# Kernel tuning notes

Measured on AMD Instinct MI355X. Metric: run time of the kernel, lower is better.

The kernel has to match this reference:

```python
import jax, jax.numpy as jnp
import numpy as np
from jax import lax

B, T, MEL, D, H, NC = 8, 256, 128, 192, 4, 20
C_EVENT, C_SCENE = 8, 64
ETA, LR, ALPHA = 0.9, 0.1, 0.01  # memory momentum, write lr, forget rate
EPS = 1e-5


def _ln(x, g, b):
    m = x.mean(-1, keepdims=True)
    v = ((x - m) ** 2).mean(-1, keepdims=True)
    return (x - m) / jnp.sqrt(v + EPS) * g + b


def _mem_step(x, t, M, S, Wk, Wv, Wq, chunk):
    # x: [B,D]; M,S: [B,D,D]. Titans-style neural memory, updated every `chunk` steps.
    k = x @ Wk
    v = x @ Wv
    q = x @ Wq
    err = v - jnp.einsum('bd,bde->be', k, M)          # surprise / prediction error
    S_new = ETA * S + LR * jnp.einsum('bd,be->bde', k, err)
    M_new = (1.0 - ALPHA) * M + S_new
    upd = (t % chunk) == 0
    S = jnp.where(upd, S_new, S)
    M = jnp.where(upd, M_new, M)
    out = jnp.einsum('bd,bde->be', q, M)              # retrieval
    return out, M, S


def setup_inputs() -> dict:
    key = jax.random.key(0)
    ks = jax.random.split(key, 24)
    w = lambda k, shp, s=0.05: jax.random.normal(k, shp, dtype=jnp.float32) * s
    inp = {
        'x': jax.random.normal(ks[0], (B, T, MEL), dtype=jnp.float32),
        'W_in': w(ks[1], (MEL, D)), 'b_in': jnp.zeros((D,), jnp.float32),
        # MHA at seq_len=1: softmax over one key -> weight 1, so only V and out proj matter
        'Wv_a': w(ks[2], (D, D)), 'bv_a': jnp.zeros((D,), jnp.float32),
        'Wo_a': w(ks[3], (D, D)), 'bo_a': jnp.zeros((D,), jnp.float32),
        # conformer conv module (degenerate seq_len=1: depthwise conv -> center tap)
        'ln1_g': jnp.ones((D,), jnp.float32), 'ln1_b': jnp.zeros((D,), jnp.float32),
        'pw1_w': w(ks[4], (D, 2 * D)), 'pw1_b': jnp.zeros((2 * D,), jnp.float32),
        'dw_w': w(ks[5], (D,), 0.2), 'dw_b': jnp.zeros((D,), jnp.float32),
        'bn_s': jnp.ones((D,), jnp.float32), 'bn_b': jnp.zeros((D,), jnp.float32),
        'pw2_w': w(ks[6], (D, D)), 'pw2_b': jnp.zeros((D,), jnp.float32),
        # theta (event) / delta (scene) neural memory projections
        'Wk_t': w(ks[7], (D, D)), 'Wv_t': w(ks[8], (D, D)), 'Wq_t': w(ks[9], (D, D)),
        'Wk_d': w(ks[10], (D, D)), 'Wv_d': w(ks[11], (D, D)), 'Wq_d': w(ks[12], (D, D)),
        'ln2_g': jnp.ones((D,), jnp.float32), 'ln2_b': jnp.zeros((D,), jnp.float32),
        'Wc': w(ks[13], (D, NC)), 'bc': jnp.zeros((NC,), jnp.float32),
    }
    return inp


def reference(x, W_in, b_in, Wv_a, bv_a, Wo_a, bo_a, ln1_g, ln1_b, pw1_w, pw1_b,
              dw_w, dw_b, bn_s, bn_b, pw2_w, pw2_b, Wk_t, Wv_t, Wq_t,
              Wk_d, Wv_d, Wq_d, ln2_g, ln2_b, Wc, bc):
    xp = x @ W_in + b_in                               # [B,T,D]

    def step(carry, inp):
        x_t, t = inp                                   # x_t: [B,D]
        Mt, St, Md, Sd = carry
        d_out, Md, Sd = _mem_step(x_t, t, Md, Sd, Wk_d, Wv_d, Wq_d, C_SCENE)
        x1 = x_t + 0.5 * d_out
        attn = (x1 @ Wv_a + bv_a) @ Wo_a + bo_a        # single-token self-attn
        x2 = x1 + attn
        h = _ln(x2, ln1_g, ln1_b)
        h = h @ pw1_w + pw1_b
        a, g = jnp.split(h, 2, axis=-1)
        h = a * jax.nn.sigmoid(g)                      # GLU
        h = h * dw_w + dw_b                            # depthwise conv center tap
        h = h * bn_s + bn_b                            # eval-mode BN
        h = jax.nn.silu(h)
        h = h @ pw2_w + pw2_b
        x3 = x2 + h
        t_out, Mt, St = _mem_step(x3, t, Mt, St, Wk_t, Wv_t, Wq_t, C_EVENT)
        x4 = x3 + 0.5 * t_out
        return (Mt, St, Md, Sd), _ln(x4, ln2_g, ln2_b)

    z = jnp.zeros((B, D, D), jnp.float32)
    xs = (jnp.swapaxes(xp, 0, 1), jnp.arange(T))       # [T,B,D], [T]
    _, ys = lax.scan(step, (z, z, z, z), xs)
    y = jnp.swapaxes(ys, 0, 1)                         # [B,T,D]
    pooled = y.mean(axis=1)
    return pooled @ Wc + bc                            # [B,NC]
```

## Files before the change

kernel.cpp:

```cpp
#include <hip/hip_runtime.h>
#include <math.h>

#define Bb 8
#define Tt 256
#define MEL 128
#define Dd 192
#define NCc 20
#define ND 4
#define NT 32
#define ETAc 0.9f
#define LRc 0.1f
#define MDEC 0.99f
#define EPSc 1e-5f
#define PT 2
#define PTILES 128
#define RTT 4
#define PADD 196

__device__ __forceinline__ float sigmoidf_(float x) {
    return 1.0f / (1.0f + __expf(-x));
}

__device__ __forceinline__ float memcoef(int n, int i) {
    float m = LRc, pw = LRc;
    for (int nn = i + 1; nn <= n; nn++) { pw *= ETAc; m = MDEC * m + pw; }
    return m;
}

__device__ __forceinline__ float dot4(float4 a, float4 b) {
    return a.x * b.x + a.y * b.y + a.z * b.z + a.w * b.w;
}

__global__ __launch_bounds__(192) void prep(
    const float* __restrict__ Wv_a, const float* __restrict__ Wo_a,
    const float* __restrict__ bv_a, const float* __restrict__ bo_a,
    const float* __restrict__ Wq_t, const float* __restrict__ Wq_d,
    const float* __restrict__ x, const float* __restrict__ W_in,
    const float* __restrict__ b_in, const float* __restrict__ Wk_d,
    const float* __restrict__ Wv_d,
    float* __restrict__ Wavo_ws, float* __restrict__ b_avo,
    float* __restrict__ WqtT, float* __restrict__ WqdT,
    float* __restrict__ Kd_ws, float* __restrict__ Vd_ws,
    float* __restrict__ pooled, unsigned int* __restrict__ cnt)
{
    __shared__ __align__(16) float smem[768];
    int blk = blockIdx.x, tid = threadIdx.x;

    if (blk < 48) {
        int m0 = blk * 4;
        for (int q = tid; q < 4 * Dd; q += 192) smem[q] = Wv_a[m0 * Dd + q];
        __syncthreads();
        int o = tid;
        float a0 = 0.f, a1 = 0.f, a2 = 0.f, a3 = 0.f;
        #pragma unroll 4
        for (int k = 0; k < Dd; k += 2) {
            float w0 = Wo_a[(k + 0) * Dd + o], w1 = Wo_a[(k + 1) * Dd + o];
            a0 += w0 * smem[0 * Dd + k] + w1 * smem[0 * Dd + k + 1];
            a1 += w0 * smem[1 * Dd + k] + w1 * smem[1 * Dd + k + 1];
            a2 += w0 * smem[2 * Dd + k] + w1 * smem[2 * Dd + k + 1];
            a3 += w0 * smem[3 * Dd + k] + w1 * smem[3 * Dd + k + 1];
        }
        Wavo_ws[(m0 + 0) * Dd + o] = a0;
        Wavo_ws[(m0 + 1) * Dd + o] = a1;
        Wavo_ws[(m0 + 2) * Dd + o] = a2;
        Wavo_ws[(m0 + 3) * Dd + o] = a3;
        return;
    }
    if (blk == 48) {
        int o = tid;
        float s = bo_a[o];
        #pragma unroll 4
        for (int m = 0; m < Dd; m++) s += bv_a[m] * Wo_a[m * Dd + o];
        b_avo[o] = s;
        return;
    }
    if (blk < 97) {
        int r0 = 4 * (blk - 49);
        float4 v;
        v.x = Wq_t[(r0 + 0) * Dd + tid];
        v.y = Wq_t[(r0 + 1) * Dd + tid];
        v.z = Wq_t[(r0 + 2) * Dd + tid];
        v.w = Wq_t[(r0 + 3) * Dd + tid];
        *(float4*)&WqtT[tid * Dd + r0] = v;
        return;
    }
    if (blk < 145) {
        int r0 = 4 * (blk - 97);
        float4 v;
        v.x = Wq_d[(r0 + 0) * Dd + tid];
        v.y = Wq_d[(r0 + 1) * Dd + tid];
        v.z = Wq_d[(r0 + 2) * Dd + tid];
        v.w = Wq_d[(r0 + 3) * Dd + tid];
        *(float4*)&WqdT[tid * Dd + r0] = v;
        return;
    }
    if (blk == 177) {
        for (int q = tid; q < Bb * Dd; q += 192) pooled[q] = 0.f;
        if (tid < 12) cnt[tid] = 0u;
        return;
    }

    int q = blk - 145;
    int b = q >> 2, i = q & 3;
    float* XR = smem;
    float* XP = smem + 128;
    if (tid < 128) XR[tid] = x[((size_t)b * Tt + 64 * i) * MEL + tid];
    __syncthreads();
    {
        int o = tid;
        float acc = b_in[o];
        #pragma unroll 8
        for (int k = 0; k < MEL; k += 4) {
            acc += W_in[(k + 0) * Dd + o] * XR[k + 0];
            acc += W_in[(k + 1) * Dd + o] * XR[k + 1];
            acc += W_in[(k + 2) * Dd + o] * XR[k + 2];
            acc += W_in[(k + 3) * Dd + o] * XR[k + 3];
        }
        XP[o] = acc;
    }
    __syncthreads();
    {
        int o = tid;
        float ak = 0.f, av = 0.f;
        #pragma unroll 4
        for (int k = 0; k < Dd; k += 4) {
            float x0 = XP[k + 0], x1 = XP[k + 1], x2 = XP[k + 2], x3 = XP[k + 3];
            ak += Wk_d[(k + 0) * Dd + o] * x0 + Wk_d[(k + 1) * Dd + o] * x1
                + Wk_d[(k + 2) * Dd + o] * x2 + Wk_d[(k + 3) * Dd + o] * x3;
            av += Wv_d[(k + 0) * Dd + o] * x0 + Wv_d[(k + 1) * Dd + o] * x1
                + Wv_d[(k + 2) * Dd + o] * x2 + Wv_d[(k + 3) * Dd + o] * x3;
        }
        Kd_ws[(b * ND + i) * Dd + o] = ak;
        Vd_ws[(b * ND + i) * Dd + o] = av;
    }
}

__global__ __launch_bounds__(192) void delta_solve(
    const float* __restrict__ WqdT, const float* __restrict__ Kd_ws,
    float* __restrict__ Vd_ws, float* __restrict__ Ud_ws)
{
    int blk = blockIdx.x, b = blk / 5, role = blk % 5, tid = threadIdx.x;
    if (role == 0) {
        __shared__ __align__(16) float K4[ND][Dd], V4[ND][Dd];
        __shared__ float G[16], mc[16];
        for (int q = tid; q < ND * 48; q += 192) {
            int i = q / 48, c = q - i * 48;
            ((float4*)K4[i])[c] = ((const float4*)&Kd_ws[(b * ND + i) * Dd])[c];
            ((float4*)V4[i])[c] = ((const float4*)&Vd_ws[(b * ND + i) * Dd])[c];
        }
        __syncthreads();
        if (tid < 16) {
            int i = tid >> 2, j = tid & 3;
            float s = 0.f;
            for (int d = 0; d < Dd; d++) s += K4[i][d] * K4[j][d];
            G[tid] = s;
            mc[tid] = (j <= i) ? memcoef(i, j) : 0.f;
        }
        __syncthreads();
        for (int i = 1; i < ND; i++) {
            float acc = V4[i][tid];
            for (int m = 0; m < i; m++)
                acc -= mc[(i - 1) * ND + m] * G[i * ND + m] * V4[m][tid];
            V4[i][tid] = acc;
            __syncthreads();
        }
        for (int i = 0; i < ND; i++) Vd_ws[(b * ND + i) * Dd + tid] = V4[i][tid];
    } else {
        __shared__ float KS[Dd];
        int i = role - 1;
        KS[tid] = Kd_ws[(b * ND + i) * Dd + tid];
        __syncthreads();
        int o = tid;
        float acc = 0.f;
        #pragma unroll 8
        for (int k = 0; k < Dd; k += 4) {
            acc += WqdT[(k + 0) * Dd + o] * KS[k + 0];
            acc += WqdT[(k + 1) * Dd + o] * KS[k + 1];
            acc += WqdT[(k + 2) * Dd + o] * KS[k + 2];
            acc += WqdT[(k + 3) * Dd + o] * KS[k + 3];
        }
        Ud_ws[(b * ND + i) * Dd + o] = acc;
    }
}

__global__ __launch_bounds__(192) void pipeline(
    const float* __restrict__ x, const float* __restrict__ W_in,
    const float* __restrict__ b_in,
    const float* __restrict__ ln1_g, const float* __restrict__ ln1_b,
    const float* __restrict__ pw1_w, const float* __restrict__ pw1_b,
    const float* __restrict__ dw_w, const float* __restrict__ dw_b,
    const float* __restrict__ bn_s, const float* __restrict__ bn_b,
    const float* __restrict__ pw2_w, const float* __restrict__ pw2_b,
    const float* __restrict__ Wavo_ws, const float* __restrict__ b_avo,
    const float* __restrict__ Ed_ws, const float* __restrict__ Ud_ws,
    float* __restrict__ x3_ws)
{
    int blk = blockIdx.x;
    int b = blk >> 7, tile = blk & 127;
    int t0 = tile * PT, n = tile >> 5;
    int tid = threadIdx.x;

    __shared__ __align__(16) float XR[PT][MEL];
    __shared__ __align__(16) float XP[PT][Dd];
    __shared__ __align__(16) float ED[ND][PADD], UD[ND][PADD];
    __shared__ __align__(16) float X1[PT][Dd], X2[PT][Dd];
    __shared__ __align__(16) float LNX[PT][Dd], HG[PT][Dd];
    __shared__ float WQs[PT * ND];
    __shared__ float mv[PT][2];

    if (tid < PT * 32) {
        int r = tid >> 5, c = tid & 31;
        ((float4*)XR[r])[c] = ((const float4*)&x[((size_t)b * Tt + t0 + r) * MEL])[c];
    }
    for (int q = tid; q < ND * 48 * 2; q += 192) {
        int which = q >= ND * 48;
        int qq = which ? q - ND * 48 : q;
        int i = qq / 48, c = qq - i * 48;
        if (!which) ((float4*)ED[i])[c] = ((const float4*)&Ed_ws[(b * ND + i) * Dd])[c];
        else        ((float4*)UD[i])[c] = ((const float4*)&Ud_ws[(b * ND + i) * Dd])[c];
    }
    __syncthreads();

    int o = tid;
    {
        float acc[PT];
        float bb = b_in[o];
        #pragma unroll
        for (int r = 0; r < PT; r++) acc[r] = bb;
        #pragma unroll 8
        for (int k = 0; k < MEL; k += 4) {
            float w0 = W_in[(k + 0) * Dd + o], w1 = W_in[(k + 1) * Dd + o];
            float w2 = W_in[(k + 2) * Dd + o], w3 = W_in[(k + 3) * Dd + o];
            #pragma unroll
            for (int r = 0; r < PT; r++) {
                float4 xv = *(const float4*)&XR[r][k];
                acc[r] += w0 * xv.x + w1 * xv.y + w2 * xv.z + w3 * xv.w;
            }
        }
        #pragma unroll
        for (int r = 0; r < PT; r++) XP[r][tid] = acc[r];
    }
    __syncthreads();

    if (tid < PT * 32) {
        int r = tid >> 5, i = (tid >> 3) & 3, c = tid & 7;
        float s = 0.f;
        const float* xp = XP[r];
        const float* u = UD[i];
        #pragma unroll
        for (int j = 0; j < 24; j++) s += xp[c * 24 + j] * u[c * 24 + j];
        s += __shfl_down(s, 4, 8);
        s += __shfl_down(s, 2, 8);
        s += __shfl_down(s, 1, 8);
        if (c == 0) {
            float coef = (i <= n) ? memcoef(n, i) : 0.f;
            WQs[r * ND + i] = s * coef;
        }
    }
    __syncthreads();

    {
        #pragma unroll
        for (int r = 0; r < PT; r++) {
            float dout = WQs[r * ND + 0] * ED[0][tid] + WQs[r * ND + 1] * ED[1][tid]
                       + WQs[r * ND + 2] * ED[2][tid] + WQs[r * ND + 3] * ED[3][tid];
            X1[r][tid] = XP[r][tid] + 0.5f * dout;
        }
    }
    __syncthreads();

    {
        float acc[PT];
        float bb = b_avo[o];
        #pragma unroll
        for (int r = 0; r < PT; r++) acc[r] = bb;
        #pragma unroll 8
        for (int k = 0; k < Dd; k += 4) {
            float w0 = Wavo_ws[(k + 0) * Dd + o], w1 = Wavo_ws[(k + 1) * Dd + o];
            float w2 = Wavo_ws[(k + 2) * Dd + o], w3 = Wavo_ws[(k + 3) * Dd + o];
            #pragma unroll
            for (int r = 0; r < PT; r++) {
                float4 xv = *(const float4*)&X1[r][k];
                acc[r] += w0 * xv.x + w1 * xv.y + w2 * xv.z + w3 * xv.w;
            }
        }
        #pragma unroll
        for (int r = 0; r < PT; r++) X2[r][tid] = X1[r][tid] + acc[r];
    }
    __syncthreads();

    if (tid < PT * 32) {
        int r = tid >> 5, j = tid & 31;
        float s = 0.f, sq = 0.f;
        for (int d = j; d < Dd; d += 32) { float v = X2[r][d]; s += v; sq += v * v; }
        for (int off = 16; off > 0; off >>= 1) {
            s += __shfl_down(s, off, 32); sq += __shfl_down(sq, off, 32);
        }
        if (j == 0) {
            float mean = s / Dd;
            mv[r][0] = mean;
            mv[r][1] = rsqrtf(sq / Dd - mean * mean + EPSc);
        }
    }
    __syncthreads();
    {
        float g = ln1_g[tid], bb = ln1_b[tid];
        #pragma unroll
        for (int r = 0; r < PT; r++)
            LNX[r][tid] = (X2[r][tid] - mv[r][0]) * mv[r][1] * g + bb;
    }
    __syncthreads();

    {
        float aa[PT], gg[PT];
        float ba = pw1_b[o], bg = pw1_b[o + Dd];
        #pragma unroll
        for (int r = 0; r < PT; r++) { aa[r] = ba; gg[r] = bg; }
        #pragma unroll 4
        for (int k = 0; k < Dd; k += 4) {
            float wa0 = pw1_w[(k + 0) * 2 * Dd + o], wg0 = pw1_w[(k + 0) * 2 * Dd + Dd + o];
            float wa1 = pw1_w[(k + 1) * 2 * Dd + o], wg1 = pw1_w[(k + 1) * 2 * Dd + Dd + o];
            float wa2 = pw1_w[(k + 2) * 2 * Dd + o], wg2 = pw1_w[(k + 2) * 2 * Dd + Dd + o];
            float wa3 = pw1_w[(k + 3) * 2 * Dd + o], wg3 = pw1_w[(k + 3) * 2 * Dd + Dd + o];
            #pragma unroll
            for (int r = 0; r < PT; r++) {
                float4 xv = *(const float4*)&LNX[r][k];
                aa[r] += wa0 * xv.x + wa1 * xv.y + wa2 * xv.z + wa3 * xv.w;
                gg[r] += wg0 * xv.x + wg1 * xv.y + wg2 * xv.z + wg3 * xv.w;
            }
        }
        float dww = dw_w[o], dwb = dw_b[o], bns = bn_s[o], bnb = bn_b[o];
        #pragma unroll
        for (int r = 0; r < PT; r++) {
            float h = aa[r] * sigmoidf_(gg[r]);
            h = h * dww + dwb;
            h = h * bns + bnb;
            h = h * sigmoidf_(h);
            HG[r][tid] = h;
        }
    }
    __syncthreads();

    {
        float acc[PT];
        float bb = pw2_b[o];
        #pragma unroll
        for (int r = 0; r < PT; r++) acc[r] = bb;
        #pragma unroll 8
        for (int k = 0; k < Dd; k += 4) {
            float w0 = pw2_w[(k + 0) * Dd + o], w1 = pw2_w[(k + 1) * Dd + o];
            float w2 = pw2_w[(k + 2) * Dd + o], w3 = pw2_w[(k + 3) * Dd + o];
            #pragma unroll
            for (int r = 0; r < PT; r++) {
                float4 xv = *(const float4*)&HG[r][k];
                acc[r] += w0 * xv.x + w1 * xv.y + w2 * xv.z + w3 * xv.w;
            }
        }
        #pragma unroll
        for (int r = 0; r < PT; r++)
            x3_ws[((size_t)b * Tt + t0 + r) * Dd + tid] = X2[r][tid] + acc[r];
    }
}

__global__ __launch_bounds__(384) void theta_projU_solve(
    const float* __restrict__ x3_ws,
    const float* __restrict__ Wk_t, const float* __restrict__ Wv_t,
    const float* __restrict__ WqtT,
    float* __restrict__ Kt_ws, float* __restrict__ Vt_ws,
    float* __restrict__ Ut_ws, unsigned int* __restrict__ cnt)
{
    int blk = blockIdx.x, b = blk >> 5, i = blk & 31;
    int tid = threadIdx.x;
    int h = (tid >= Dd) ? 1 : 0;
    int o = tid - h * Dd;
    __shared__ __align__(16) float XS[Dd];
    __shared__ __align__(16) float KS[Dd];
    __shared__ __align__(16) float PS[Dd];

    if (tid < 48)
        ((float4*)XS)[tid] = ((const float4*)&x3_ws[((size_t)b * Tt + 8 * i) * Dd])[tid];
    __syncthreads();

    const float* W = h ? Wv_t : Wk_t;
    float a = 0.f;
    #pragma unroll 4
    for (int k = 0; k < Dd; k += 4) {
        a += W[(k + 0) * Dd + o] * XS[k + 0] + W[(k + 1) * Dd + o] * XS[k + 1]
           + W[(k + 2) * Dd + o] * XS[k + 2] + W[(k + 3) * Dd + o] * XS[k + 3];
    }
    if (!h) { Kt_ws[(b * NT + i) * Dd + o] = a; KS[o] = a; }
    else    { Vt_ws[(b * NT + i) * Dd + o] = a; }
    __syncthreads();

    float au = 0.f;
    int k0 = h * 96;
    #pragma unroll 4
    for (int k = k0; k < k0 + 96; k += 4) {
        au += WqtT[(k + 0) * Dd + o] * KS[k + 0] + WqtT[(k + 1) * Dd + o] * KS[k + 1]
            + WqtT[(k + 2) * Dd + o] * KS[k + 2] + WqtT[(k + 3) * Dd + o] * KS[k + 3];
    }
    if (h) PS[o] = au;
    __syncthreads();
    if (!h) Ut_ws[(b * NT + i) * Dd + o] = au + PS[o];

    __syncthreads();
    __shared__ unsigned int sdone;
    if (tid == 0) { __threadfence(); sdone = atomicAdd(&cnt[b], 1u); }
    __syncthreads();
    if (sdone != 31u) return;
    __threadfence();

    __shared__ __align__(16) float K[NT][PADD];
    __shared__ float A[NT * NT], mc[NT * NT];

    for (int q = tid; q < NT * 48; q += 384) {
        int ii = q / 48, c = q - ii * 48;
        ((float4*)K[ii])[c] = ((const float4*)&Kt_ws[(b * NT + ii) * Dd])[c];
    }
    if (tid < NT) {
        int ii = tid;
        float m = 0.f, pw = LRc;
        for (int nn = 0; nn < NT; nn++) {
            float v;
            if (nn < ii) v = 0.f;
            else if (nn == ii) { m = LRc; v = m; }
            else { pw *= ETAc; m = MDEC * m + pw; v = m; }
            mc[nn * NT + ii] = v;
        }
    }
    __syncthreads();
    for (int p = tid; p < NT * NT; p += 384) {
        int ii = p >> 5, j = p & 31;
        float s = 0.f;
        if (j < ii) {
            const float4* ki = (const float4*)K[ii];
            const float4* kj = (const float4*)K[j];
            float g = 0.f;
            #pragma unroll 4
            for (int kk = 0; kk < 48; kk++) g += dot4(ki[kk], kj[kk]);
            s = mc[(ii - 1) * NT + j] * g;
        }
        A[p] = s;
    }
    __syncthreads();
    if (tid < Dd) {
        float e[NT];
        #pragma unroll
        for (int ii = 0; ii < NT; ii++) e[ii] = Vt_ws[(b * NT + ii) * Dd + tid];
        #pragma unroll
        for (int ii = 1; ii < NT; ii++) {
            float acc = e[ii];
            #pragma unroll
            for (int m = 0; m < ii; m++) acc -= A[ii * NT + m] * e[m];
            e[ii] = acc;
        }
        #pragma unroll
        for (int ii = 0; ii < NT; ii++) Vt_ws[(b * NT + ii) * Dd + tid] = e[ii];
    }
}

__global__ __launch_bounds__(256) void retrieve(
    const float* __restrict__ x3_ws, const float* __restrict__ Ut_ws,
    const float* __restrict__ Et_ws, const float* __restrict__ ln2_g,
    const float* __restrict__ ln2_b, float* __restrict__ pooled,
    const float* __restrict__ Wc, const float* __restrict__ bc,
    float* __restrict__ out, unsigned int* __restrict__ cnt)
{
    int blk = blockIdx.x, b = blk >> 6, tile = blk & 63;
    int t0 = tile * RTT, n = tile >> 1;
    int tid = threadIdx.x;

    __shared__ __align__(16) float UT[NT][PADD];
    __shared__ __align__(16) float XS[RTT][PADD];
    __shared__ float WQ[RTT * NT];
    __shared__ float mv[RTT][2];

    for (int q = tid; q < NT * 48; q += 256) {
        int i = q / 48, c = q - i * 48;
        ((float4*)UT[i])[c] = ((const float4*)&Ut_ws[(b * NT + i) * Dd])[c];
    }
    for (int q = tid; q < RTT * 48; q += 256) {
        int r = q / 48, c = q - r * 48;
        ((float4*)XS[r])[c] = ((const float4*)&x3_ws[((size_t)b * Tt + t0 + r) * Dd])[c];
    }
    __syncthreads();

    {
        int r = tid >> 6, i = (tid >> 1) & 31, h = tid & 1;
        const float4* u4 = (const float4*)UT[i];
        const float4* x4 = (const float4*)XS[r];
        float s = 0.f;
        #pragma unroll 8
        for (int kk = h * 24; kk < h * 24 + 24; kk++) s += dot4(u4[kk], x4[kk]);
        s += __shfl_down(s, 1, 2);
        if (h == 0) {
            float coef = (i <= n) ? memcoef(n, i) : 0.f;
            WQ[r * NT + i] = s * coef;
        }
    }
    __syncthreads();

    if (tid < Dd) {
        float acc[RTT] = {};
        #pragma unroll 4
        for (int i = 0; i < NT; i++) {
            float e = Et_ws[(b * NT + i) * Dd + tid];
            #pragma unroll
            for (int r = 0; r < RTT; r++) acc[r] += WQ[r * NT + i] * e;
        }
        #pragma unroll
        for (int r = 0; r < RTT; r++) XS[r][tid] += 0.5f * acc[r];
    }
    __syncthreads();

    if (tid < RTT * 32) {
        int r = tid >> 5, j = tid & 31;
        float s = 0.f, sq = 0.f;
        for (int d = j; d < Dd; d += 32) { float v = XS[r][d]; s += v; sq += v * v; }
        for (int off = 16; off > 0; off >>= 1) {
            s += __shfl_down(s, off, 32); sq += __shfl_down(sq, off, 32);
        }
        if (j == 0) {
            float mean = s / Dd;
            mv[r][0] = mean;
            mv[r][1] = rsqrtf(sq / Dd - mean * mean + EPSc);
        }
    }
    __syncthreads();

    if (tid < Dd) {
        float g = ln2_g[tid], bb = ln2_b[tid];
        float sum = 0.f;
        #pragma unroll
        for (int r = 0; r < RTT; r++)
            sum += (XS[r][tid] - mv[r][0]) * mv[r][1] * g + bb;
        atomicAdd(&pooled[b * Dd + tid], sum);
    }

    __syncthreads();
    __shared__ unsigned int sdone;
    if (tid == 0) { __threadfence(); sdone = atomicAdd(&cnt[8], 1u); }
    __syncthreads();
    if (sdone != (unsigned)(Bb * 64 - 1)) return;
    __threadfence();

    if (tid < Bb * NCc) {
        int b2 = tid / NCc, c = tid - b2 * NCc;
        float s = 0.f;
        for (int d = 0; d < Dd; d++) s += pooled[b2 * Dd + d] * Wc[d * NCc + c];
        out[tid] = s * (1.0f / Tt) + bc[c];
    }
}

extern "C" void kernel_launch(void* const* d_in, const int* in_sizes, int n_in,
                              void* d_out, int out_size, void* d_ws, size_t ws_size,
                              hipStream_t stream) {
    const float* x     = (const float*)d_in[0];
    const float* W_in  = (const float*)d_in[1];
    const float* b_in  = (const float*)d_in[2];
    const float* Wv_a  = (const float*)d_in[3];
    const float* bv_a  = (const float*)d_in[4];
    const float* Wo_a  = (const float*)d_in[5];
    const float* bo_a  = (const float*)d_in[6];
    const float* ln1_g = (const float*)d_in[7];
    const float* ln1_b = (const float*)d_in[8];
    const float* pw1_w = (const float*)d_in[9];
    const float* pw1_b = (const float*)d_in[10];
    const float* dw_w  = (const float*)d_in[11];
    const float* dw_b  = (const float*)d_in[12];
    const float* bn_s  = (const float*)d_in[13];
    const float* bn_b  = (const float*)d_in[14];
    const float* pw2_w = (const float*)d_in[15];
    const float* pw2_b = (const float*)d_in[16];
    const float* Wk_t  = (const float*)d_in[17];
    const float* Wv_t  = (const float*)d_in[18];
    const float* Wq_t  = (const float*)d_in[19];
    const float* Wk_d  = (const float*)d_in[20];
    const float* Wv_d  = (const float*)d_in[21];
    const float* Wq_d  = (const float*)d_in[22];
    const float* ln2_g = (const float*)d_in[23];
    const float* ln2_b = (const float*)d_in[24];
    const float* Wc    = (const float*)d_in[25];
    const float* bc    = (const float*)d_in[26];

    float* ws = (float*)d_ws;
    size_t off = 0;
    float* x3_ws   = ws + off; off += (size_t)Bb * Tt * Dd;
    float* Kd_ws   = ws + off; off += Bb * ND * Dd;
    float* Vd_ws   = ws + off; off += Bb * ND * Dd;
    float* Ud_ws   = ws + off; off += Bb * ND * Dd;
    float* Kt_ws   = ws + off; off += Bb * NT * Dd;
    float* Vt_ws   = ws + off; off += Bb * NT * Dd;
    float* Ut_ws   = ws + off; off += Bb * NT * Dd;
    float* pooled  = ws + off; off += Bb * Dd;
    float* Wavo_ws = ws + off; off += Dd * Dd;
    float* WqtT    = ws + off; off += Dd * Dd;
    float* WqdT    = ws + off; off += Dd * Dd;
    float* b_avo   = ws + off; off += Dd;
    unsigned int* cnt = (unsigned int*)(ws + off); off += 16;

    prep<<<178, 192, 0, stream>>>(
        Wv_a, Wo_a, bv_a, bo_a, Wq_t, Wq_d,
        x, W_in, b_in, Wk_d, Wv_d,
        Wavo_ws, b_avo, WqtT, WqdT, Kd_ws, Vd_ws, pooled, cnt);
    delta_solve<<<Bb * 5, 192, 0, stream>>>(WqdT, Kd_ws, Vd_ws, Ud_ws);
    pipeline<<<Bb * PTILES, 192, 0, stream>>>(
        x, W_in, b_in, ln1_g, ln1_b, pw1_w, pw1_b, dw_w, dw_b,
        bn_s, bn_b, pw2_w, pw2_b, Wavo_ws, b_avo, Vd_ws, Ud_ws, x3_ws);
    theta_projU_solve<<<Bb * NT, 384, 0, stream>>>(
        x3_ws, Wk_t, Wv_t, WqtT, Kt_ws, Vt_ws, Ut_ws, cnt);
    retrieve<<<Bb * 64, 256, 0, stream>>>(
        x3_ws, Ut_ws, Vt_ws, ln2_g, ln2_b, pooled, Wc, bc, (float*)d_out, cnt);
}
```

Before: 202.0 us.

## Fuse theta projection and solve into pipeline kernel via precomputed Wk_t·Wq_t product

Result: slower. 290.9 us (+44.0%).

```diff
diff --git a/kernel.cpp b/kernel.cpp
--- a/kernel.cpp
+++ b/kernel.cpp
@@ -41,7 +41,7 @@
     float* __restrict__ Wavo_ws, float* __restrict__ b_avo,
     float* __restrict__ WqtT, float* __restrict__ WqdT,
     float* __restrict__ Kd_ws, float* __restrict__ Vd_ws,
-    float* __restrict__ pooled, unsigned int* __restrict__ cnt)
+    float* __restrict__ pooled, unsigned* __restrict__ cnt)
 {
     __shared__ __align__(16) float smem[768];
     int blk = blockIdx.x, tid = threadIdx.x;
@@ -137,9 +137,33 @@
 
 __global__ __launch_bounds__(192) void delta_solve(
     const float* __restrict__ WqdT, const float* __restrict__ Kd_ws,
-    float* __restrict__ Vd_ws, float* __restrict__ Ud_ws)
+    float* __restrict__ Vd_ws, float* __restrict__ Ud_ws,
+    const float* __restrict__ Wk_t, const float* __restrict__ WqtT,
+    float* __restrict__ WqkT)
 {
-    int blk = blockIdx.x, b = blk / 5, role = blk % 5, tid = threadIdx.x;
+    int blk = blockIdx.x, tid = threadIdx.x;
+    if (blk >= 40) {
+        __shared__ __align__(16) float RK[4 * Dd];
+        int d0 = 4 * (blk - 40);
+        for (int q = tid; q < 4 * Dd; q += 192) RK[q] = Wk_t[d0 * Dd + q];
+        __syncthreads();
+        int o = tid;
+        float a0 = 0.f, a1 = 0.f, a2 = 0.f, a3 = 0.f;
+        #pragma unroll 4
+        for (int k = 0; k < Dd; k += 2) {
+            float w0 = WqtT[(k + 0) * Dd + o], w1 = WqtT[(k + 1) * Dd + o];
+            a0 += w0 * RK[0 * Dd + k] + w1 * RK[0 * Dd + k + 1];
+            a1 += w0 * RK[1 * Dd + k] + w1 * RK[1 * Dd + k + 1];
+            a2 += w0 * RK[2 * Dd + k] + w1 * RK[2 * Dd + k + 1];
+            a3 += w0 * RK[3 * Dd + k] + w1 * RK[3 * Dd + k + 1];
+        }
+        WqkT[(d0 + 0) * Dd + o] = a0;
+        WqkT[(d0 + 1) * Dd + o] = a1;
+        WqkT[(d0 + 2) * Dd + o] = a2;
+        WqkT[(d0 + 3) * Dd + o] = a3;
+        return;
+    }
+    int b = blk / 5, role = blk % 5;
     if (role == 0) {
         __shared__ __align__(16) float K4[ND][Dd], V4[ND][Dd];
         __shared__ float G[16], mc[16];
@@ -149,11 +173,19 @@
             ((float4*)V4[i])[c] = ((const float4*)&Vd_ws[(b * ND + i) * Dd])[c];
         }
         __syncthreads();
+        if (tid < 128) {
+            int p = tid >> 3, c = tid & 7;
+            int i = p >> 2, j = p & 3;
+            float s = 0.f;
+            #pragma unroll
+            for (int d = c * 24; d < c * 24 + 24; d++) s += K4[i][d] * K4[j][d];
+            s += __shfl_down(s, 4, 8);
+            s += __shfl_down(s, 2, 8);
+            s += __shfl_down(s, 1, 8);
+            if (c == 0) G[p] = s;
+        }
         if (tid < 16) {
             int i = tid >> 2, j = tid & 3;
-            float s = 0.f;
-            for (int d = 0; d < Dd; d++) s += K4[i][d] * K4[j][d];
-            G[tid] = s;
             mc[tid] = (j <= i) ? memcoef(i, j) : 0.f;
         }
         __syncthreads();
@@ -193,7 +225,11 @@
     const float* __restrict__ pw2_w, const float* __restrict__ pw2_b,
     const float* __restrict__ Wavo_ws, const float* __restrict__ b_avo,
     const float* __restrict__ Ed_ws, const float* __restrict__ Ud_ws,
-    float* __restrict__ x3_ws)
+    const float* __restrict__ Wk_t, const float* __restrict__ Wv_t,
+    const float* __restrict__ WqkT,
+    float* __restrict__ x3_ws,
+    float* __restrict__ Kt_ws, float* __restrict__ Vt_ws,
+    float* __restrict__ Ut_ws, unsigned* __restrict__ cnt)
 {
     int blk = blockIdx.x;
     int b = blk >> 7, tile = blk & 127;
@@ -207,6 +243,7 @@
     __shared__ __align__(16) float LNX[PT][Dd], HG[PT][Dd];
     __shared__ float WQs[PT * ND];
     __shared__ float mv[PT][2];
+    __shared__ float As[NT * NT];
 
     if (tid < PT * 32) {
         int r = tid >> 5, c = tid & 31;
@@ -341,6 +378,7 @@
     }
     __syncthreads();
 
+    float x3v0;
     {
         float acc[PT];
         float bb = pw2_b[o];
@@ -359,91 +397,49 @@
         #pragma unroll
         for (int r = 0; r < PT; r++)
             x3_ws[((size_t)b * Tt + t0 + r) * Dd + tid] = X2[r][tid] + acc[r];
-    }
-}
-
-__global__ __launch_bounds__(384) void theta_projU_solve(
-    const float* __restrict__ x3_ws,
-    const float* __restrict__ Wk_t, const float* __restrict__ Wv_t,
-    const float* __restrict__ WqtT,
-    float* __restrict__ Kt_ws, float* __restrict__ Vt_ws,
-    float* __restrict__ Ut_ws, unsigned int* __restrict__ cnt)
-{
-    int blk = blockIdx.x, b = blk >> 5, i = blk & 31;
-    int tid = threadIdx.x;
-    int h = (tid >= Dd) ? 1 : 0;
-    int o = tid - h * Dd;
-    __shared__ __align__(16) float XS[Dd];
-    __shared__ __align__(16) float KS[Dd];
-    __shared__ __align__(16) float PS[Dd];
-
-    if (tid < 48)
-        ((float4*)XS)[tid] = ((const float4*)&x3_ws[((size_t)b * Tt + 8 * i) * Dd])[tid];
-    __syncthreads();
-
-    const float* W = h ? Wv_t : Wk_t;
-    float a = 0.f;
-    #pragma unroll 4
-    for (int k = 0; k < Dd; k += 4) {
-        a += W[(k + 0) * Dd + o] * XS[k + 0] + W[(k + 1) * Dd + o] * XS[k + 1]
-           + W[(k + 2) * Dd + o] * XS[k + 2] + W[(k + 3) * Dd + o] * XS[k + 3];
-    }
-    if (!h) { Kt_ws[(b * NT + i) * Dd + o] = a; KS[o] = a; }
-    else    { Vt_ws[(b * NT + i) * Dd + o] = a; }
-    __syncthreads();
-
-    float au = 0.f;
-    int k0 = h * 96;
-    #pragma unroll 4
-    for (int k = k0; k < k0 + 96; k += 4) {
-        au += WqtT[(k + 0) * Dd + o] * KS[k + 0] + WqtT[(k + 1) * Dd + o] * KS[k + 1]
-            + WqtT[(k + 2) * Dd + o] * KS[k + 2] + WqtT[(k + 3) * Dd + o] * KS[k + 3];
-    }
-    if (h) PS[o] = au;
-    __syncthreads();
-    if (!h) Ut_ws[(b * NT + i) * Dd + o] = au + PS[o];
-
-    __syncthreads();
-    __shared__ unsigned int sdone;
-    if (tid == 0) { __threadfence(); sdone = atomicAdd(&cnt[b], 1u); }
-    __syncthreads();
-    if (sdone != 31u) return;
-    __threadfence();
-
-    __shared__ __align__(16) float K[NT][PADD];
-    __shared__ float A[NT * NT], mc[NT * NT];
-
-    for (int q = tid; q < NT * 48; q += 384) {
-        int ii = q / 48, c = q - ii * 48;
-        ((float4*)K[ii])[c] = ((const float4*)&Kt_ws[(b * NT + ii) * Dd])[c];
-    }
-    if (tid < NT) {
-        int ii = tid;
-        float m = 0.f, pw = LRc;
-        for (int nn = 0; nn < NT; nn++) {
-            float v;
-            if (nn < ii) v = 0.f;
-            else if (nn == ii) { m = LRc; v = m; }
-            else { pw *= ETAc; m = MDEC * m + pw; v = m; }
-            mc[nn * NT + ii] = v;
-        }
-    }
-    __syncthreads();
-    for (int p = tid; p < NT * NT; p += 384) {
-        int ii = p >> 5, j = p & 31;
-        float s = 0.f;
-        if (j < ii) {
-            const float4* ki = (const float4*)K[ii];
-            const float4* kj = (const float4*)K[j];
-            float g = 0.f;
-            #pragma unroll 4
-            for (int kk = 0; kk < 48; kk++) g += dot4(ki[kk], kj[kk]);
-            s = mc[(ii - 1) * NT + j] * g;
-        }
-        A[p] = s;
-    }
-    __syncthreads();
-    if (tid < Dd) {
+        x3v0 = X2[0][tid] + acc[0];
+    }
+
+    if ((tile & 3) == 0) {
+        int i = tile >> 2;
+        float* XS = LNX[0];
+        XS[tid] = x3v0;
+        __syncthreads();
+
+        float ak = 0.f, av = 0.f, au = 0.f;
+        #pragma unroll 4
+        for (int k = 0; k < Dd; k += 2) {
+            float x0 = XS[k + 0], x1 = XS[k + 1];
+            ak += Wk_t[(k + 0) * Dd + o] * x0 + Wk_t[(k + 1) * Dd + o] * x1;
+            av += Wv_t[(k + 0) * Dd + o] * x0 + Wv_t[(k + 1) * Dd + o] * x1;
+            au += WqkT[(k + 0) * Dd + o] * x0 + WqkT[(k + 1) * Dd + o] * x1;
+        }
+        Kt_ws[(b * NT + i) * Dd + o] = ak;
+        Vt_ws[(b * NT + i) * Dd + o] = av;
+        Ut_ws[(b * NT + i) * Dd + o] = au;
+
+        __syncthreads();
+        __shared__ unsigned sdone;
+        if (tid == 0) { __threadfence(); sdone = atomicAdd(&cnt[b], 1u); }
+        __syncthreads();
+        if (sdone != 31u) return;
+        __threadfence();
+
+        const float* Kb = &Kt_ws[(size_t)b * NT * Dd];
+        for (int p = tid; p < NT * NT; p += 192) {
+            int ii = p >> 5, j = p & 31;
+            float s = 0.f;
+            if (j < ii) {
+                const float4* ki = (const float4*)(Kb + ii * Dd);
+                const float4* kj = (const float4*)(Kb + j * Dd);
+                float g = 0.f;
+                #pragma unroll 4
+                for (int kk = 0; kk < 48; kk++) g += dot4(ki[kk], kj[kk]);
+                s = memcoef(ii - 1, j) * g;
+            }
+            As[p] = s;
+        }
+        __syncthreads();
         float e[NT];
         #pragma unroll
         for (int ii = 0; ii < NT; ii++) e[ii] = Vt_ws[(b * NT + ii) * Dd + tid];
@@ -451,7 +447,7 @@
         for (int ii = 1; ii < NT; ii++) {
             float acc = e[ii];
             #pragma unroll
-            for (int m = 0; m < ii; m++) acc -= A[ii * NT + m] * e[m];
+            for (int m = 0; m < ii; m++) acc -= As[ii * NT + m] * e[m];
             e[ii] = acc;
         }
         #pragma unroll
@@ -464,7 +460,7 @@
     const float* __restrict__ Et_ws, const float* __restrict__ ln2_g,
     const float* __restrict__ ln2_b, float* __restrict__ pooled,
     const float* __restrict__ Wc, const float* __restrict__ bc,
-    float* __restrict__ out, unsigned int* __restrict__ cnt)
+    float* __restrict__ out, unsigned* __restrict__ cnt)
 {
     int blk = blockIdx.x, b = blk >> 6, tile = blk & 63;
     int t0 = tile * RTT, n = tile >> 1;
@@ -538,7 +534,7 @@
     }
 
     __syncthreads();
-    __shared__ unsigned int sdone;
+    __shared__ unsigned sdone;
     if (tid == 0) { __threadfence(); sdone = atomicAdd(&cnt[8], 1u); }
     __syncthreads();
     if (sdone != (unsigned)(Bb * 64 - 1)) return;
@@ -596,19 +592,20 @@
     float* Wavo_ws = ws + off; off += Dd * Dd;
     float* WqtT    = ws + off; off += Dd * Dd;
     float* WqdT    = ws + off; off += Dd * Dd;
+    float* WqkT    = ws + off; off += Dd * Dd;
     float* b_avo   = ws + off; off += Dd;
-    unsigned int* cnt = (unsigned int*)(ws + off); off += 16;
+    unsigned* cnt  = (unsigned*)(ws + off); off += 16;
 
     prep<<<178, 192, 0, stream>>>(
         Wv_a, Wo_a, bv_a, bo_a, Wq_t, Wq_d,
         x, W_in, b_in, Wk_d, Wv_d,
         Wavo_ws, b_avo, WqtT, WqdT, Kd_ws, Vd_ws, pooled, cnt);
-    delta_solve<<<Bb * 5, 192, 0, stream>>>(WqdT, Kd_ws, Vd_ws, Ud_ws);
+    delta_solve<<<88, 192, 0, stream>>>(
+        WqdT, Kd_ws, Vd_ws, Ud_ws, Wk_t, WqtT, WqkT);
     pipeline<<<Bb * PTILES, 192, 0, stream>>>(
         x, W_in, b_in, ln1_g, ln1_b, pw1_w, pw1_b, dw_w, dw_b,
-        bn_s, bn_b, pw2_w, pw2_b, Wavo_ws, b_avo, Vd_ws, Ud_ws, x3_ws);
-    theta_projU_solve<<<Bb * NT, 384, 0, stream>>>(
-        x3_ws, Wk_t, Wv_t, WqtT, Kt_ws, Vt_ws, Ut_ws, cnt);
+        bn_s, bn_b, pw2_w, pw2_b, Wavo_ws, b_avo, Vd_ws, Ud_ws,
+        Wk_t, Wv_t, WqkT, x3_ws, Kt_ws, Vt_ws, Ut_ws, cnt);
     retrieve<<<Bb * 64, 256, 0, stream>>>(
         x3_ws, Ut_ws, Vt_ws, ln2_g, ln2_b, pooled, Wc, bc, (float*)d_out, cnt);
 }
```
